# Kernel optimization log

Hardware: AMD Instinct MI355X
Metric: run time of the kernel (lower is better)

## Reference

```python
import jax
import jax.numpy as jnp
from jax import lax
import numpy as np

DIM = 64
EPS = 1e-5
DN = ('NCDHW', 'OIDHW', 'NCDHW')


def setup_inputs() -> dict:
    key = jax.random.key(0)
    ks = jax.random.split(key, 4)
    x = jax.random.normal(ks[0], (2, DIM, 64, 64, 64), dtype=jnp.float32)
    gamma = jnp.ones((DIM,), jnp.float32)
    beta = jnp.zeros((DIM,), jnp.float32)
    w0 = jax.random.normal(ks[1], (DIM, 1, 5, 5, 5), jnp.float32) * 0.1
    b0 = jnp.zeros((DIM,), jnp.float32)
    ws = jax.random.normal(ks[2], (DIM, 1, 7, 7, 7), jnp.float32) * 0.05
    bs = jnp.zeros((DIM,), jnp.float32)
    w1 = jax.random.normal(ks[3], (DIM, DIM, 1, 1, 1), jnp.float32) * 0.1
    b1 = jnp.zeros((DIM,), jnp.float32)
    return {"x": x, "gamma": gamma, "beta": beta, "w0": w0, "b0": b0,
            "ws": ws, "bs": bs, "w1": w1, "b1": b1}


def _cb(b):
    # broadcast per-channel vector over NCDHW
    return b.reshape(1, -1, 1, 1, 1)


def reference(x, gamma, beta, w0, b0, ws, bs, w1, b1):
    dim = x.shape[1]
    # BatchNorm (training mode, biased variance) over N, D, H, W per channel
    mean = jnp.mean(x, axis=(0, 2, 3, 4), keepdims=True)
    var = jnp.var(x, axis=(0, 2, 3, 4), keepdims=True)
    xn = (x - mean) * lax.rsqrt(var + EPS) * _cb(gamma) + _cb(beta)
    # depthwise conv3d k=5, pad=2 (same)
    attn = lax.conv_general_dilated(xn, w0, (1, 1, 1), [(2, 2)] * 3,
                                    feature_group_count=dim,
                                    dimension_numbers=DN) + _cb(b0)
    # dilated depthwise conv3d k=7, dilation=3, pad=9 (same)
    attn = lax.conv_general_dilated(attn, ws, (1, 1, 1), [(9, 9)] * 3,
                                    rhs_dilation=(3, 3, 3),
                                    feature_group_count=dim,
                                    dimension_numbers=DN) + _cb(bs)
    # pointwise 1x1x1 conv
    attn = lax.conv_general_dilated(attn, w1, (1, 1, 1), [(0, 0)] * 3,
                                    dimension_numbers=DN) + _cb(b1)
    # gated multiply with residual input (u = x.clone())
    return x * attn
```

## Files before the change

### kernel.cpp

```cpp
#include <hip/hip_runtime.h>
#include <math.h>

#define C_DIM 64
#define N_B 2
#define SPATIAL (64*64*64)
#define PLANE_SZ (64*64)
#define EPSV 1e-5f

__global__ __launch_bounds__(256) void k_stats(const float* __restrict__ x,
                                               float* __restrict__ wsf) {
    int c = blockIdx.x >> 4;
    int part = blockIdx.x & 15;
    int tid = threadIdx.x;
    const int per_part = SPATIAL / 16;
    float s = 0.f, sq = 0.f;
    for (int n = 0; n < N_B; ++n) {
        const float* base = x + ((size_t)(n * C_DIM + c)) * SPATIAL + (size_t)part * per_part;
        const float4* b4 = (const float4*)base;
        #pragma unroll
        for (int it = 0; it < 16; ++it) {
            float4 v = b4[it * 256 + tid];
            s  += v.x + v.y + v.z + v.w;
            sq += v.x*v.x + v.y*v.y + v.z*v.z + v.w*v.w;
        }
    }
    __shared__ float rs[256], rq[256];
    rs[tid] = s; rq[tid] = sq;
    __syncthreads();
    for (int off = 128; off > 0; off >>= 1) {
        if (tid < off) { rs[tid] += rs[tid+off]; rq[tid] += rq[tid+off]; }
        __syncthreads();
    }
    if (tid == 0) {
        atomicAdd(&wsf[c], rs[0]);
        atomicAdd(&wsf[64 + c], rq[0]);
    }
}

__global__ void k_finalize(float* __restrict__ wsf,
                           const float* __restrict__ gamma,
                           const float* __restrict__ beta) {
    int c = threadIdx.x;
    float cnt = (float)(N_B * SPATIAL);
    float mean = wsf[c] / cnt;
    float var = wsf[64 + c] / cnt - mean * mean;
    float sc = gamma[c] * rsqrtf(var + EPSV);
    wsf[128 + c] = sc;
    wsf[192 + c] = beta[c] - mean * sc;
}

#define K2D 12
#define K2H 12
#define K2W 36
__global__ __launch_bounds__(256) void k_conv5(const float* __restrict__ x,
                                               const float* __restrict__ w0,
                                               const float* __restrict__ b0,
                                               const float* __restrict__ wsf,
                                               float* __restrict__ attn0) {
    __shared__ float sh[K2D * K2H * K2W];
    __shared__ float wt[125];
    int tid = threadIdx.x;
    int tx = tid & 31;
    int ty = tid >> 5;
    int wtile = blockIdx.x;
    int dt = blockIdx.y & 7;
    int ht = blockIdx.y >> 3;
    int nc = blockIdx.z;
    int c = nc & 63;
    int w0i = wtile * 32;
    int h0 = ht * 8;
    int d0 = dt * 8;
    const float* xb = x + (size_t)nc * SPATIAL;
    float sc = wsf[128 + c], shv = wsf[192 + c];
    if (tid < 125) wt[tid] = w0[c * 125 + tid];
    for (int idx = tid; idx < K2D * K2H * K2W; idx += 256) {
        int z = idx / (K2H * K2W);
        int rem = idx - z * (K2H * K2W);
        int y = rem / K2W;
        int xw = rem - y * K2W;
        int gd = d0 - 2 + z, gh = h0 - 2 + y, gw = w0i - 2 + xw;
        float v = 0.f;
        if ((unsigned)gd < 64u && (unsigned)gh < 64u && (unsigned)gw < 64u)
            v = xb[(size_t)gd * PLANE_SZ + gh * 64 + gw] * sc + shv;
        sh[idx] = v;
    }
    __syncthreads();
    float acc[8] = {0,0,0,0,0,0,0,0};
    #pragma unroll
    for (int z = 0; z < 12; ++z) {
        #pragma unroll
        for (int j = 0; j < 5; ++j) {
            #pragma unroll
            for (int k = 0; k < 5; ++k) {
                float v = sh[(z * K2H + (ty + j)) * K2W + tx + k];
                #pragma unroll
                for (int i = 0; i < 5; ++i) {
                    int dz = z - i;
                    if (dz >= 0 && dz < 8)
                        acc[dz] += wt[(i * 5 + j) * 5 + k] * v;
                }
            }
        }
    }
    float bias = b0[c];
    float* ob = attn0 + (size_t)nc * SPATIAL + (size_t)(h0 + ty) * 64 + w0i + tx;
    #pragma unroll
    for (int dz = 0; dz < 8; ++dz)
        ob[(size_t)(d0 + dz) * PLANE_SZ] = acc[dz] + bias;
}

#define ROWS7 26
#define COLS7 84
#define S7_ELEMS (ROWS7 * COLS7)
#define S7_ITERS 5

template<int P>
__device__ __forceinline__ void conv7_stage(const float* __restrict__ ab,
                                            const float* __restrict__ wc,
                                            float* __restrict__ sh,
                                            int tid, int hh, int w,
                                            int j0, int rd,
                                            const int (&goff)[S7_ITERS],
                                            const float (&gmsk)[S7_ITERS],
                                            float (&acc)[8]) {
    int m = j0 - 3 + P;
    int z = 3 * m + rd;
    bool zok = (m >= 0) && (z < 64);
    __syncthreads();
    if (zok) {
        const float* pb = ab + (size_t)z * PLANE_SZ;
        #pragma unroll
        for (int k = 0; k < S7_ITERS; ++k)
            sh[k * 512 + tid] = pb[goff[k]] * gmsk[k];
    }
    __syncthreads();
    if (zok) {
        #pragma unroll
        for (int v = 0; v < 7; ++v) {
            float val[7];
            int rb = (hh + 3 * v) * COLS7 + w;
            #pragma unroll
            for (int u = 0; u < 7; ++u) val[u] = sh[rb + 3 * u];
            #pragma unroll
            for (int t = 0; t < 7; ++t) {
                const int q = P - t;
                if (q >= 0 && q < 8) {
                    #pragma unroll
                    for (int u = 0; u < 7; ++u)
                        acc[q] = fmaf(wc[t * 49 + v * 7 + u], val[u], acc[q]);
                }
            }
        }
    }
}

__global__ __launch_bounds__(512) void k_conv7(const float* __restrict__ attn0,
                                               const float* __restrict__ wsv,
                                               const float* __restrict__ bs,
                                               float* __restrict__ attn1) {
    __shared__ float sh[S7_ITERS * 512];
    int tid = threadIdx.x;
    int w = tid & 63;
    int hh = tid >> 6;
    int ht = blockIdx.x;
    int rd = blockIdx.y % 3;
    int j0 = (blockIdx.y / 3) * 8;
    int nc = blockIdx.z;
    int c = nc & 63;
    int h0 = ht * 8;
    int h = h0 + hh;
    const float* ab = attn0 + (size_t)nc * SPATIAL;
    const float* wc = wsv + c * 343;

    int goff[S7_ITERS];
    float gmsk[S7_ITERS];
    #pragma unroll
    for (int k = 0; k < S7_ITERS; ++k) {
        int idx = k * 512 + tid;
        int row = idx / COLS7;
        int col = idx - row * COLS7;
        int gy = h0 - 9 + row;
        int gx = col - 9;
        bool valid = (idx < S7_ELEMS) && (col < 82) &&
                     ((unsigned)gy < 64u) && ((unsigned)gx < 64u);
        goff[k] = valid ? (gy * 64 + gx) : 0;
        gmsk[k] = valid ? 1.f : 0.f;
    }

    float acc[8] = {0,0,0,0,0,0,0,0};

    conv7_stage< 0>(ab, wc, sh, tid, hh, w, j0, rd, goff, gmsk, acc);
    conv7_stage< 1>(ab, wc, sh, tid, hh, w, j0, rd, goff, gmsk, acc);
    conv7_stage< 2>(ab, wc, sh, tid, hh, w, j0, rd, goff, gmsk, acc);
    conv7_stage< 3>(ab, wc, sh, tid, hh, w, j0, rd, goff, gmsk, acc);
    conv7_stage< 4>(ab, wc, sh, tid, hh, w, j0, rd, goff, gmsk, acc);
    conv7_stage< 5>(ab, wc, sh, tid, hh, w, j0, rd, goff, gmsk, acc);
    conv7_stage< 6>(ab, wc, sh, tid, hh, w, j0, rd, goff, gmsk, acc);
    conv7_stage< 7>(ab, wc, sh, tid, hh, w, j0, rd, goff, gmsk, acc);
    conv7_stage< 8>(ab, wc, sh, tid, hh, w, j0, rd, goff, gmsk, acc);
    conv7_stage< 9>(ab, wc, sh, tid, hh, w, j0, rd, goff, gmsk, acc);
    conv7_stage<10>(ab, wc, sh, tid, hh, w, j0, rd, goff, gmsk, acc);
    conv7_stage<11>(ab, wc, sh, tid, hh, w, j0, rd, goff, gmsk, acc);
    conv7_stage<12>(ab, wc, sh, tid, hh, w, j0, rd, goff, gmsk, acc);
    conv7_stage<13>(ab, wc, sh, tid, hh, w, j0, rd, goff, gmsk, acc);

    float bias = bs[c];
    float* ob = attn1 + (size_t)nc * SPATIAL + (size_t)h * 64 + w;
    #pragma unroll
    for (int q = 0; q < 8; ++q) {
        int d = 3 * (j0 + q) + rd;
        if (d < 64)
            ob[(size_t)d * PLANE_SZ] = acc[q] + bias;
    }
}

__global__ __launch_bounds__(256) void k_pointwise(const float* __restrict__ attn1,
                                                   const float* __restrict__ x,
                                                   const float* __restrict__ w1,
                                                   const float* __restrict__ b1,
                                                   float* __restrict__ out) {
    __shared__ float at[64 * 64];
    int tid = threadIdx.x;
    int sl = tid & 63;
    int cg = __builtin_amdgcn_readfirstlane(tid >> 6);
    int s0 = blockIdx.x * 64;
    int n = blockIdx.y;
    const float* a_base = attn1 + (size_t)n * C_DIM * SPATIAL + s0;
    #pragma unroll
    for (int it = 0; it < 16; ++it) {
        int idx = it * 256 + tid;
        int row = idx >> 6;
        at[idx] = a_base[(size_t)row * SPATIAL + sl];
    }
    __syncthreads();
    float acc[16];
    #pragma unroll
    for (int j = 0; j < 16; ++j) acc[j] = 0.f;
    for (int ci = 0; ci < 64; ++ci) {
        float va = at[ci * 64 + sl];
        #pragma unroll
        for (int j = 0; j < 16; ++j) {
            int cc = cg * 16 + j;
            acc[j] += w1[cc * 64 + ci] * va;
        }
    }
    const float* xb = x + (size_t)n * C_DIM * SPATIAL + s0;
    float* ob = out + (size_t)n * C_DIM * SPATIAL + s0;
    #pragma unroll
    for (int j = 0; j < 16; ++j) {
        int cc = cg * 16 + j;
        float attn = acc[j] + b1[cc];
        ob[(size_t)cc * SPATIAL + sl] = xb[(size_t)cc * SPATIAL + sl] * attn;
    }
}

extern "C" void kernel_launch(void* const* d_in, const int* in_sizes, int n_in,
                              void* d_out, int out_size, void* d_ws, size_t ws_size,
                              hipStream_t stream) {
    const float* x     = (const float*)d_in[0];
    const float* gamma = (const float*)d_in[1];
    const float* beta  = (const float*)d_in[2];
    const float* w0    = (const float*)d_in[3];
    const float* b0    = (const float*)d_in[4];
    const float* wsv   = (const float*)d_in[5];
    const float* bs    = (const float*)d_in[6];
    const float* w1    = (const float*)d_in[7];
    const float* b1    = (const float*)d_in[8];
    float* out = (float*)d_out;
    float* wsf = (float*)d_ws;
    float* attn1 = wsf + 256;

    hipMemsetAsync(d_ws, 0, 1024, stream);
    k_stats<<<dim3(1024), dim3(256), 0, stream>>>(x, wsf);
    k_finalize<<<dim3(1), dim3(64), 0, stream>>>(wsf, gamma, beta);
    k_conv5<<<dim3(2, 64, 128), dim3(256), 0, stream>>>(x, w0, b0, wsf, out);
    k_conv7<<<dim3(8, 9, 128), dim3(512), 0, stream>>>(out, wsv, bs, attn1);
    k_pointwise<<<dim3(4096, 2), dim3(256), 0, stream>>>(attn1, x, w1, b1, out);
}
```

Before: 1.192 ms.

## Double-buffer dilated conv7 shared-memory planes to overlap loads with compute

The dilated 7x7x7 depthwise conv now keeps two shared-memory plane buffers. Each stage issues the global loads for the next z-plane into registers before computing on the current plane, then stores them to the other buffer. This cuts the per-stage barriers from two to one and hides global load latency behind the FMAs. In exchange it doubles LDS use per block, adds registers for the prefetch, and sets a launch-bounds occupancy hint that may force register spills.

```diff
diff --git a/kernel.cpp b/kernel.cpp
--- a/kernel.cpp
+++ b/kernel.cpp
@@ -113,6 +113,7 @@
 #define COLS7 84
 #define S7_ELEMS (ROWS7 * COLS7)
 #define S7_ITERS 5
+#define S7_BUF 2560
 
 template<int P>
 __device__ __forceinline__ void conv7_stage(const float* __restrict__ ab,
@@ -123,24 +124,29 @@
                                             const int (&goff)[S7_ITERS],
                                             const float (&gmsk)[S7_ITERS],
                                             float (&acc)[8]) {
-    int m = j0 - 3 + P;
-    int z = 3 * m + rd;
-    bool zok = (m >= 0) && (z < 64);
-    __syncthreads();
-    if (zok) {
-        const float* pb = ab + (size_t)z * PLANE_SZ;
+    float* cur = sh + (P & 1) * S7_BUF;
+    float* nxt = sh + ((P + 1) & 1) * S7_BUF;
+    int mP = j0 - 3 + P;
+    int zP = 3 * mP + rd;
+    bool zokP = (mP >= 0) && (zP < 64);
+    int mN = mP + 1;
+    int zN = zP + 3;
+    bool zokN = (P < 13) && (mN >= 0) && (zN < 64);
+
+    float r[S7_ITERS];
+    if (zokN) {
+        const float* pb = ab + (size_t)zN * PLANE_SZ;
         #pragma unroll
         for (int k = 0; k < S7_ITERS; ++k)
-            sh[k * 512 + tid] = pb[goff[k]] * gmsk[k];
-    }
-    __syncthreads();
-    if (zok) {
+            r[k] = pb[goff[k]];
+    }
+    if (zokP) {
         #pragma unroll
         for (int v = 0; v < 7; ++v) {
             float val[7];
             int rb = (hh + 3 * v) * COLS7 + w;
             #pragma unroll
-            for (int u = 0; u < 7; ++u) val[u] = sh[rb + 3 * u];
+            for (int u = 0; u < 7; ++u) val[u] = cur[rb + 3 * u];
             #pragma unroll
             for (int t = 0; t < 7; ++t) {
                 const int q = P - t;
@@ -152,13 +158,19 @@
             }
         }
     }
-}
-
-__global__ __launch_bounds__(512) void k_conv7(const float* __restrict__ attn0,
-                                               const float* __restrict__ wsv,
-                                               const float* __restrict__ bs,
-                                               float* __restrict__ attn1) {
-    __shared__ float sh[S7_ITERS * 512];
+    if (zokN) {
+        #pragma unroll
+        for (int k = 0; k < S7_ITERS; ++k)
+            nxt[k * 512 + tid] = r[k] * gmsk[k];
+    }
+    __syncthreads();
+}
+
+__global__ __launch_bounds__(512, 8) void k_conv7(const float* __restrict__ attn0,
+                                                  const float* __restrict__ wsv,
+                                                  const float* __restrict__ bs,
+                                                  float* __restrict__ attn1) {
+    __shared__ float sh[2 * S7_BUF];
     int tid = threadIdx.x;
     int w = tid & 63;
     int hh = tid >> 6;
@@ -185,6 +197,18 @@
                      ((unsigned)gy < 64u) && ((unsigned)gx < 64u);
         goff[k] = valid ? (gy * 64 + gx) : 0;
         gmsk[k] = valid ? 1.f : 0.f;
+    }
+
+    {
+        int m0 = j0 - 3;
+        int z0 = 3 * m0 + rd;
+        if (m0 >= 0 && z0 < 64) {
+            const float* pb = ab + (size_t)z0 * PLANE_SZ;
+            #pragma unroll
+            for (int k = 0; k < S7_ITERS; ++k)
+                sh[k * 512 + tid] = pb[goff[k]] * gmsk[k];
+        }
+        __syncthreads();
     }
 
     float acc[8] = {0,0,0,0,0,0,0,0};
```

Result: slower. 1.280 ms (+7.4%).
